# Kernel optimization log

Hardware: AMD Instinct MI355X
Metric: run time of the kernel (lower is better)

Reference implementation:

```python
import jax, jax.numpy as jnp
import numpy as np


def setup_inputs() -> dict:
    key = jax.random.key(0)
    k1, k2 = jax.random.split(key)
    N, C, D, Hg, Wg = 2, 12, 8, 16, 16
    H, W = 1024, 1024
    grid = jax.random.normal(k1, (N, C, D, Hg, Wg), dtype=jnp.float32)
    guidemap = jax.random.uniform(k2, (N, 1, H, W), dtype=jnp.float32)
    return {"grid": grid, "guidemap": guidemap}


def reference(grid, guidemap):
    # Bilateral grid slicing: 3D trilinear grid_sample, padding='border', align_corners=True.
    # grid: [N, C, D, Hg, Wg]; guidemap: [N, 1, H, W] -> out: [N, C, H, W]
    N, C, D, Hg, Wg = grid.shape
    _, _, H, W = guidemap.shape

    # Normalized sample coords in [-1, 1] (meshgrid over output pixels).
    yn = jnp.linspace(-1.0, 1.0, H)                      # [H]
    xn = jnp.linspace(-1.0, 1.0, W)                      # [W]
    zn = guidemap[:, 0] * 2.0 - 1.0                      # [N, H, W]

    # Unnormalize (align_corners=True) and clamp to border.
    iy = jnp.clip((yn + 1.0) * 0.5 * (Hg - 1), 0.0, Hg - 1.0)  # [H]
    ix = jnp.clip((xn + 1.0) * 0.5 * (Wg - 1), 0.0, Wg - 1.0)  # [W]
    iz = jnp.clip((zn + 1.0) * 0.5 * (D - 1), 0.0, D - 1.0)    # [N, H, W]

    iy0 = jnp.floor(iy).astype(jnp.int32)
    ix0 = jnp.floor(ix).astype(jnp.int32)
    iy1 = jnp.minimum(iy0 + 1, Hg - 1)
    ix1 = jnp.minimum(ix0 + 1, Wg - 1)
    wy = (iy - iy0)[:, None]                              # [H, 1]
    wx = (ix - ix0)[None, :]                              # [1, W]

    Y0, Y1 = iy0[:, None], iy1[:, None]                   # [H, 1]
    X0, X1 = ix0[None, :], ix1[None, :]                   # [1, W]

    iz0 = jnp.floor(iz).astype(jnp.int32)                 # [N, H, W]
    iz1 = jnp.minimum(iz0 + 1, D - 1)
    wz = iz - iz0                                         # [N, H, W]

    def sample_one(g, z0, z1, wzn):
        # g: [C, D, Hg, Wg]; z0, z1, wzn: [H, W]
        def gat(zz, yy, xx):
            return g[:, zz, yy, xx]                       # [C, H, W]
        # interpolate along z first, then x, then y
        c00 = gat(z0, Y0, X0) * (1.0 - wzn) + gat(z1, Y0, X0) * wzn
        c01 = gat(z0, Y0, X1) * (1.0 - wzn) + gat(z1, Y0, X1) * wzn
        c10 = gat(z0, Y1, X0) * (1.0 - wzn) + gat(z1, Y1, X0) * wzn
        c11 = gat(z0, Y1, X1) * (1.0 - wzn) + gat(z1, Y1, X1) * wzn
        c0 = c00 * (1.0 - wx) + c01 * wx
        c1 = c10 * (1.0 - wx) + c11 * wx
        return c0 * (1.0 - wy) + c1 * wy                  # [C, H, W]

    coeff = jax.vmap(sample_one)(grid, iz0, iz1, wz)      # [N, C, H, W]
    return coeff
```

## Files before the change

### kernel.cpp

```cpp
#include <hip/hip_runtime.h>

#define H 1024
#define W 1024
#define NC 12
#define ND 8
#define HG 16
#define WG 16
#define ROWS 2

__global__ __launch_bounds__(256, 4) void slice_kernel(
    const float* __restrict__ grid,
    const float* __restrict__ guide,
    float* __restrict__ out)
{
    const int y0  = blockIdx.x * ROWS;
    const int n   = blockIdx.y;
    const int tid = threadIdx.x;
    const int xb  = tid * 4;

    const float* gd = guide + ((size_t)n * H + y0) * W;
    float4 g4[ROWS];
    g4[0] = *(const float4*)&gd[xb];
    g4[1] = *(const float4*)&gd[W + xb];

    __shared__ __align__(16) float sg[ROWS][WG * ND * NC];
    const float* gbase = grid + (size_t)n * NC * ND * HG * WG;

    #pragma unroll
    for (int r = 0; r < ROWS; ++r) {
        const int y = y0 + r;
        float yn = -1.0f + (float)y * (2.0f / (float)(H - 1));
        float iy = (yn + 1.0f) * 0.5f * (float)(HG - 1);
        iy = fminf(fmaxf(iy, 0.0f), (float)(HG - 1));
        int   iy0 = (int)floorf(iy);
        int   iy1 = min(iy0 + 1, HG - 1);
        float wy  = iy - (float)iy0;

        for (int i = tid; i < WG * ND * NC; i += 256) {
            int x  = i & (WG - 1);
            int zc = i >> 4;
            int z  = zc & (ND - 1);
            int c  = zc >> 3;
            const float* gp = gbase + ((c * ND + z) * HG) * WG + x;
            float r0 = gp[iy0 * WG];
            float r1 = gp[iy1 * WG];
            sg[r][(x * ND + z) * NC + c] = r0 + (r1 - r0) * wy;
        }
    }

    int   B0[4], B1[4];
    float wxv[4];
    #pragma unroll
    for (int p = 0; p < 4; ++p) {
        const int x = xb + p;
        float xn = -1.0f + (float)x * (2.0f / (float)(W - 1));
        float ix = (xn + 1.0f) * 0.5f * (float)(WG - 1);
        ix = fminf(fmaxf(ix, 0.0f), (float)(WG - 1));
        int   ix0 = (int)floorf(ix);
        int   ix1 = min(ix0 + 1, WG - 1);
        wxv[p] = ix - (float)ix0;
        B0[p]  = ix0 * (ND * NC);
        B1[p]  = ix1 * (ND * NC);
    }

    __syncthreads();

    float* ob = out + ((size_t)n * NC * H + y0) * W;

    #pragma unroll
    for (int r = 0; r < ROWS; ++r) {
        const float gz[4] = { g4[r].x, g4[r].y, g4[r].z, g4[r].w };

        int   A00[4], A01[4], A10[4], A11[4];
        float wzv[4];
        #pragma unroll
        for (int p = 0; p < 4; ++p) {
            float zn = gz[p] * 2.0f - 1.0f;
            float iz = (zn + 1.0f) * 0.5f * (float)(ND - 1);
            iz = fminf(fmaxf(iz, 0.0f), (float)(ND - 1));
            int   iz0 = (int)floorf(iz);
            int   iz1 = min(iz0 + 1, ND - 1);
            wzv[p] = iz - (float)iz0;
            const int Z0 = iz0 * NC;
            const int Z1 = iz1 * NC;
            A00[p] = B0[p] + Z0;  A01[p] = B0[p] + Z1;
            A10[p] = B1[p] + Z0;  A11[p] = B1[p] + Z1;
        }

        #pragma unroll
        for (int cc = 0; cc < NC; cc += 4) {
            float4 q[4];
            #pragma unroll
            for (int p = 0; p < 4; ++p) {
                const float wz = wzv[p], wx = wxv[p];
                const float4 a0 = *(const float4*)&sg[r][A00[p] + cc];
                const float4 a1 = *(const float4*)&sg[r][A01[p] + cc];
                const float4 b0 = *(const float4*)&sg[r][A10[p] + cc];
                const float4 b1 = *(const float4*)&sg[r][A11[p] + cc];

                float za, zb;
                za = a0.x + (a1.x - a0.x) * wz;
                zb = b0.x + (b1.x - b0.x) * wz;
                q[p].x = za + (zb - za) * wx;

                za = a0.y + (a1.y - a0.y) * wz;
                zb = b0.y + (b1.y - b0.y) * wz;
                q[p].y = za + (zb - za) * wx;

                za = a0.z + (a1.z - a0.z) * wz;
                zb = b0.z + (b1.z - b0.z) * wz;
                q[p].z = za + (zb - za) * wx;

                za = a0.w + (a1.w - a0.w) * wz;
                zb = b0.w + (b1.w - b0.w) * wz;
                q[p].w = za + (zb - za) * wx;
            }
            {
                float4 v;
                v = make_float4(q[0].x, q[1].x, q[2].x, q[3].x);
                *(float4*)&ob[(size_t)(cc + 0) * H * W + (size_t)r * W + xb] = v;
                v = make_float4(q[0].y, q[1].y, q[2].y, q[3].y);
                *(float4*)&ob[(size_t)(cc + 1) * H * W + (size_t)r * W + xb] = v;
                v = make_float4(q[0].z, q[1].z, q[2].z, q[3].z);
                *(float4*)&ob[(size_t)(cc + 2) * H * W + (size_t)r * W + xb] = v;
                v = make_float4(q[0].w, q[1].w, q[2].w, q[3].w);
                *(float4*)&ob[(size_t)(cc + 3) * H * W + (size_t)r * W + xb] = v;
            }
        }
    }
}

extern "C" void kernel_launch(void* const* d_in, const int* in_sizes, int n_in,
                              void* d_out, int out_size, void* d_ws, size_t ws_size,
                              hipStream_t stream) {
    const float* grid  = (const float*)d_in[0];
    const float* guide = (const float*)d_in[1];
    float* out = (float*)d_out;

    dim3 grd(H / ROWS, 2);
    dim3 blk(256);
    slice_kernel<<<grd, blk, 0, stream>>>(grid, guide, out);
}
```

Baseline: 119.3 us.

## Split rows across two blocks, pad shared grid pitch, precompute bilinear weights

Each block now covers half a row pair, so every thread handles 2 pixels instead of 4 and the grid doubles in block count. The shared-memory x pitch is padded to 100 floats to reduce bank conflicts. The z/x lerps are replaced by four precomputed bilinear weights, and the occupancy hint rises to 6. This exposes more parallelism and fewer conflicts, but every block now repeats the y-interpolation preload of the grid slice, and stores become narrower float2 writes.

Measured after the change: 119.6 us. About the same (+0.3%).

```diff
diff --git a/kernel.cpp b/kernel.cpp
--- a/kernel.cpp
+++ b/kernel.cpp
@@ -7,23 +7,28 @@
 #define HG 16
 #define WG 16
 #define ROWS 2
+#define PX 2
+#define HALFW 512
+#define XPITCH 100
 
-__global__ __launch_bounds__(256, 4) void slice_kernel(
+__global__ __launch_bounds__(256, 6) void slice_kernel(
     const float* __restrict__ grid,
     const float* __restrict__ guide,
     float* __restrict__ out)
 {
-    const int y0  = blockIdx.x * ROWS;
+    const int xh  = blockIdx.x & 1;
+    const int yp  = blockIdx.x >> 1;
     const int n   = blockIdx.y;
+    const int y0  = yp * ROWS;
     const int tid = threadIdx.x;
-    const int xb  = tid * 4;
+    const int xb  = xh * HALFW + tid * PX;
 
     const float* gd = guide + ((size_t)n * H + y0) * W;
-    float4 g4[ROWS];
-    g4[0] = *(const float4*)&gd[xb];
-    g4[1] = *(const float4*)&gd[W + xb];
+    float2 g2[ROWS];
+    g2[0] = *(const float2*)&gd[xb];
+    g2[1] = *(const float2*)&gd[W + xb];
 
-    __shared__ __align__(16) float sg[ROWS][WG * ND * NC];
+    __shared__ __align__(16) float sg[ROWS][WG * XPITCH];
     const float* gbase = grid + (size_t)n * NC * ND * HG * WG;
 
     #pragma unroll
@@ -36,7 +41,9 @@
         int   iy1 = min(iy0 + 1, HG - 1);
         float wy  = iy - (float)iy0;
 
-        for (int i = tid; i < WG * ND * NC; i += 256) {
+        #pragma unroll
+        for (int k = 0; k < (WG * ND * NC) / 256; ++k) {
+            int i  = tid + k * 256;
             int x  = i & (WG - 1);
             int zc = i >> 4;
             int z  = zc & (ND - 1);
@@ -44,14 +51,14 @@
             const float* gp = gbase + ((c * ND + z) * HG) * WG + x;
             float r0 = gp[iy0 * WG];
             float r1 = gp[iy1 * WG];
-            sg[r][(x * ND + z) * NC + c] = r0 + (r1 - r0) * wy;
+            sg[r][x * XPITCH + z * NC + c] = r0 + (r1 - r0) * wy;
         }
     }
 
-    int   B0[4], B1[4];
-    float wxv[4];
+    int   B0[PX], B1[PX];
+    float wxv[PX];
     #pragma unroll
-    for (int p = 0; p < 4; ++p) {
+    for (int p = 0; p < PX; ++p) {
         const int x = xb + p;
         float xn = -1.0f + (float)x * (2.0f / (float)(W - 1));
         float ix = (xn + 1.0f) * 0.5f * (float)(WG - 1);
@@ -59,72 +66,66 @@
         int   ix0 = (int)floorf(ix);
         int   ix1 = min(ix0 + 1, WG - 1);
         wxv[p] = ix - (float)ix0;
-        B0[p]  = ix0 * (ND * NC);
-        B1[p]  = ix1 * (ND * NC);
+        B0[p]  = ix0 * XPITCH;
+        B1[p]  = ix1 * XPITCH;
     }
 
     __syncthreads();
 
-    float* ob = out + ((size_t)n * NC * H + y0) * W;
+    float* ob = out + (size_t)n * NC * H * W + (size_t)y0 * W + xb;
 
     #pragma unroll
     for (int r = 0; r < ROWS; ++r) {
-        const float gz[4] = { g4[r].x, g4[r].y, g4[r].z, g4[r].w };
+        const float gz[PX] = { g2[r].x, g2[r].y };
 
-        int   A00[4], A01[4], A10[4], A11[4];
-        float wzv[4];
+        int   A00[PX], A01[PX], A10[PX], A11[PX];
+        float w00[PX], w01[PX], w10[PX], w11[PX];
         #pragma unroll
-        for (int p = 0; p < 4; ++p) {
+        for (int p = 0; p < PX; ++p) {
             float zn = gz[p] * 2.0f - 1.0f;
             float iz = (zn + 1.0f) * 0.5f * (float)(ND - 1);
             iz = fminf(fmaxf(iz, 0.0f), (float)(ND - 1));
             int   iz0 = (int)floorf(iz);
             int   iz1 = min(iz0 + 1, ND - 1);
-            wzv[p] = iz - (float)iz0;
+            float wz  = iz - (float)iz0;
+
             const int Z0 = iz0 * NC;
             const int Z1 = iz1 * NC;
             A00[p] = B0[p] + Z0;  A01[p] = B0[p] + Z1;
             A10[p] = B1[p] + Z0;  A11[p] = B1[p] + Z1;
+
+            const float wx = wxv[p];
+            const float ux = 1.0f - wx;
+            const float uz = 1.0f - wz;
+            w00[p] = ux * uz;  w01[p] = ux * wz;
+            w10[p] = wx * uz;  w11[p] = wx * wz;
         }
 
         #pragma unroll
         for (int cc = 0; cc < NC; cc += 4) {
-            float4 q[4];
+            float4 q[PX];
             #pragma unroll
-            for (int p = 0; p < 4; ++p) {
-                const float wz = wzv[p], wx = wxv[p];
+            for (int p = 0; p < PX; ++p) {
                 const float4 a0 = *(const float4*)&sg[r][A00[p] + cc];
                 const float4 a1 = *(const float4*)&sg[r][A01[p] + cc];
                 const float4 b0 = *(const float4*)&sg[r][A10[p] + cc];
                 const float4 b1 = *(const float4*)&sg[r][A11[p] + cc];
-
-                float za, zb;
-                za = a0.x + (a1.x - a0.x) * wz;
-                zb = b0.x + (b1.x - b0.x) * wz;
-                q[p].x = za + (zb - za) * wx;
-
-                za = a0.y + (a1.y - a0.y) * wz;
-                zb = b0.y + (b1.y - b0.y) * wz;
-                q[p].y = za + (zb - za) * wx;
-
-                za = a0.z + (a1.z - a0.z) * wz;
-                zb = b0.z + (b1.z - b0.z) * wz;
-                q[p].z = za + (zb - za) * wx;
-
-                za = a0.w + (a1.w - a0.w) * wz;
-                zb = b0.w + (b1.w - b0.w) * wz;
-                q[p].w = za + (zb - za) * wx;
+                const float k00 = w00[p], k01 = w01[p], k10 = w10[p], k11 = w11[p];
+                q[p].x = a0.x * k00 + a1.x * k01 + b0.x * k10 + b1.x * k11;
+                q[p].y = a0.y * k00 + a1.y * k01 + b0.y * k10 + b1.y * k11;
+                q[p].z = a0.z * k00 + a1.z * k01 + b0.z * k10 + b1.z * k11;
+                q[p].w = a0.w * k00 + a1.w * k01 + b0.w * k10 + b1.w * k11;
             }
             {
-                float4 v;
-                v = make_float4(q[0].x, q[1].x, q[2].x, q[3].x);
-                *(float4*)&ob[(size_t)(cc + 0) * H * W + (size_t)r * W + xb] = v;
-                v = make_float4(q[0].y, q[1].y, q[2].y, q[3].y);
-                *(float4*)&ob[(size_t)(cc + 1) * H * W + (size_t)r * W + xb] = v;
-                v = make_float4(q[0].z, q[1].z, q[2].z, q[3].z);
-                *(float4*)&ob[(size_t)(cc + 2) * H * W + (size_t)r * W + xb] = v;
-                v = make_float4(q[0].w, q[1].w, q[2].w, q[3].w);
-                *(float4*)&ob[(size_t)(cc + 3) * H * W + (size_t)r * W + xb] = v;
+                float2 v;
+                v = make_float2(q[0].x, q[1].x);
+                *(float2*)&ob[(size_t)(cc + 0) * H * W + (size_t)r * W] = v;
+                v = make_float2(q[0].y, q[1].y);
+                *(float2*)&ob[(size_t)(cc + 1) * H * W + (size_t)r * W] = v;
+                v = make_float2(q[0].z, q[1].z);
+                *(float2*)&ob[(size_t)(cc + 2) * H * W + (size_t)r * W] = v;
+                v = make_float2(q[0].w, q[1].w);
+                *(float2*)&ob[(size_t)(cc + 3) * H * W + (size_t)r * W] = v;
             }
         }
     }
@@ -137,7 +138,7 @@
     const float* guide = (const float*)d_in[1];
     float* out = (float*)d_out;
 
-    dim3 grd(H / ROWS, 2);
+    dim3 grd((W / HALFW) * (H / ROWS), 2);
     dim3 blk(256);
     slice_kernel<<<grd, blk, 0, stream>>>(grid, guide, out);
 }
```
